# Kernel tuning notes

Hardware: AMD Instinct MI355X
Metric: run time of the kernel (lower is better)

## Reference

```python
import jax, jax.numpy as jnp
import numpy as np

B, S, D, T = 64, 1024, 768, 10
IS = int(S * 0.3)   # 307, token-mix inner dim
ID = int(D * 0.3)   # 230, channel-mix inner dim
EPS = 1e-5


def _cond_ln(x, embed, tid):
    # LayerNorm over last dim (no affine), then per-sample gamma/beta
    mu = jnp.mean(x, axis=-1, keepdims=True)
    var = jnp.mean(jnp.square(x - mu), axis=-1, keepdims=True)
    out = (x - mu) / jnp.sqrt(var + EPS)
    gb = embed[tid]                      # [B, 2D]
    gamma, beta = gb[:, :D], gb[:, D:]
    return gamma[:, None, :] * out + beta[:, None, :]


def setup_inputs() -> dict:
    key = jax.random.key(0)
    ks = jax.random.split(key, 8)
    x = jax.random.normal(ks[0], (B, S, D), dtype=jnp.float32)
    tasks_id = jax.random.randint(ks[1], (B,), 0, T)
    # conditional LN embeddings: gamma ~ N(1, 0.02), beta = 0
    cln1 = jnp.concatenate([1.0 + 0.02 * jax.random.normal(ks[2], (T, D)),
                            jnp.zeros((T, D))], axis=1).astype(jnp.float32)
    cln2 = jnp.concatenate([1.0 + 0.02 * jax.random.normal(ks[3], (T, D)),
                            jnp.zeros((T, D))], axis=1).astype(jnp.float32)
    # per-task weights stored [T, fout, fin] (kaiming-ish scale)
    w1_tok = jax.random.normal(ks[4], (T, IS, S), dtype=jnp.float32) * (2.0 / S) ** 0.5
    w2_tok = jax.random.normal(ks[5], (T, S, IS), dtype=jnp.float32) * (2.0 / IS) ** 0.5
    w1_ch = jax.random.normal(ks[6], (T, ID, D), dtype=jnp.float32) * (2.0 / D) ** 0.5
    w2_ch = jax.random.normal(ks[7], (T, D, ID), dtype=jnp.float32) * (2.0 / ID) ** 0.5
    return {"x": x, "tasks_id": tasks_id, "cln1": cln1, "cln2": cln2,
            "w1_tok": w1_tok, "w2_tok": w2_tok, "w1_ch": w1_ch, "w2_ch": w2_ch}


def reference(x, tasks_id, cln1, cln2, w1_tok, w2_tok, w1_ch, w2_ch):
    tid = tasks_id
    # --- token-mixing block (axis=1 ConditionalLinear) ---
    h = _cond_ln(x, cln1, tid)
    h = jnp.einsum('bnd,bcn->bcd', h, w1_tok[tid])   # [B, IS, D]
    h = jax.nn.gelu(h, approximate=False)
    h = jnp.einsum('bnd,bcn->bcd', h, w2_tok[tid])   # [B, S, D]
    x = x + h
    # --- channel-mixing block (axis=2 ConditionalLinear) ---
    h = _cond_ln(x, cln2, tid)
    h = jnp.einsum('bnd,bcd->bnc', h, w1_ch[tid])    # [B, S, ID]
    h = jax.nn.gelu(h, approximate=False)
    h = jnp.einsum('bnd,bcd->bnc', h, w2_ch[tid])    # [B, S, D]
    x = x + h
    return x
```

## Files before the change

### kernel.cpp

```cpp
#include <hip/hip_runtime.h>
#include <math.h>

typedef __bf16 bf16x8 __attribute__((ext_vector_type(8)));
typedef __bf16 bf16x4 __attribute__((ext_vector_type(4)));
typedef float  f32x4  __attribute__((ext_vector_type(4)));

constexpr int Bc = 64, Sc = 1024, Dc = 768;
constexpr int ISc = 307, IDc = 230;
constexpr int ISp = 384, IDp = 256;

static __device__ __forceinline__ float bf2f(unsigned short u) {
    return __builtin_bit_cast(float, (unsigned)u << 16);
}
static __device__ __forceinline__ float gelu_f(float v) {
    return 0.5f * v * (1.0f + erff(v * 0.70710678118654752f));
}

static __device__ __forceinline__ void gload16(const void* g, void* l) {
    __builtin_amdgcn_global_load_lds(
        (const __attribute__((address_space(1))) void*)g,
        (__attribute__((address_space(3))) void*)l, 16, 0, 0);
}

constexpr int CH0 = 10 * ISp * (Sc  / 8);
constexpr int CH1 = 10 * Sc  * (ISp / 8);
constexpr int CH2 = 10 * IDp * (Dc  / 8);
constexpr int CH3 = 10 * Dc  * (IDp / 8);
constexpr int CB0 = CH0, CB1 = CB0 + CH1, CB2 = CB1 + CH2, CB3 = CB2 + CH3;

__device__ __forceinline__ void cvt_one(
    const float* __restrict__ in, __bf16* __restrict__ out,
    int inrows, int outrows, int incols, int outcols, int c)
{
    const int cpr  = outcols >> 3;
    const int perT = outrows * cpr;
    const int t    = c / perT;
    const int rem  = c - t * perT;
    const int r    = rem / cpr;
    const int cc   = (rem - r * cpr) * 8;
    bf16x8 o;
    if (r < inrows) {
        const float* src = in + ((long)t * inrows + r) * incols + cc;
        #pragma unroll
        for (int e = 0; e < 8; e++)
            o[e] = (cc + e < incols) ? (__bf16)src[e] : (__bf16)0.0f;
    } else {
        #pragma unroll
        for (int e = 0; e < 8; e++) o[e] = (__bf16)0.0f;
    }
    *reinterpret_cast<bf16x8*>(out + ((long)t * outrows + r) * outcols + cc) = o;
}

__global__ __launch_bounds__(256) void cvt_all(
    const float* __restrict__ w1t, const float* __restrict__ w2t,
    const float* __restrict__ w1c, const float* __restrict__ w2c,
    __bf16* __restrict__ o1t, __bf16* __restrict__ o2t,
    __bf16* __restrict__ o1c, __bf16* __restrict__ o2c)
{
    const int c = blockIdx.x * 256 + threadIdx.x;
    if (c < CB0)      cvt_one(w1t, o1t, ISc, ISp, Sc,  Sc,  c);
    else if (c < CB1) cvt_one(w2t, o2t, Sc,  Sc,  ISc, ISp, c - CB0);
    else if (c < CB2) cvt_one(w1c, o1c, IDc, IDp, Dc,  Dc,  c - CB1);
    else if (c < CB3) cvt_one(w2c, o2c, Dc,  Dc,  IDc, IDp, c - CB2);
}

__global__ __launch_bounds__(256) void ln1_t(
    const float* __restrict__ x, const int* __restrict__ tasks,
    const float* __restrict__ cln, __bf16* __restrict__ h1T)
{
    constexpr int RPB = 32, LDT = Dc + 8;
    __shared__ unsigned short T[RPB * LDT];
    const int b   = blockIdx.y;
    const int t   = tasks[b];
    const int s0  = blockIdx.x * RPB;
    const int tid = threadIdx.x;
    const int wv  = tid >> 6;
    const int l   = tid & 63;

    const float4* Ga = reinterpret_cast<const float4*>(cln + (long)t * 2 * Dc);
    const float4* Be = reinterpret_cast<const float4*>(cln + (long)t * 2 * Dc + Dc);
    const float4 g0 = Ga[l], g1 = Ga[l + 64], g2 = Ga[l + 128];
    const float4 b0 = Be[l], b1 = Be[l + 64], b2 = Be[l + 128];

    #pragma unroll
    for (int rr = 0; rr < 8; rr++) {
        const int r = wv * 8 + rr;
        const float4* xr = reinterpret_cast<const float4*>(x + ((long)b * Sc + s0 + r) * Dc);
        const float4 v0 = xr[l], v1 = xr[l + 64], v2 = xr[l + 128];
        float s = v0.x + v0.y + v0.z + v0.w + v1.x + v1.y + v1.z + v1.w
                + v2.x + v2.y + v2.z + v2.w;
        float q = v0.x*v0.x + v0.y*v0.y + v0.z*v0.z + v0.w*v0.w
                + v1.x*v1.x + v1.y*v1.y + v1.z*v1.z + v1.w*v1.w
                + v2.x*v2.x + v2.y*v2.y + v2.z*v2.z + v2.w*v2.w;
        #pragma unroll
        for (int o = 1; o < 64; o <<= 1) { s += __shfl_xor(s, o); q += __shfl_xor(q, o); }
        const float mu   = s * (1.0f / Dc);
        const float var  = fmaxf(q * (1.0f / Dc) - mu * mu, 0.0f);
        const float rstd = 1.0f / sqrtf(var + 1e-5f);
        unsigned short* tr = &T[r * LDT];
        bf16x4 o0, o1, o2;
        o0[0] = (__bf16)(g0.x * ((v0.x - mu) * rstd) + b0.x);
        o0[1] = (__bf16)(g0.y * ((v0.y - mu) * rstd) + b0.y);
        o0[2] = (__bf16)(g0.z * ((v0.z - mu) * rstd) + b0.z);
        o0[3] = (__bf16)(g0.w * ((v0.w - mu) * rstd) + b0.w);
        o1[0] = (__bf16)(g1.x * ((v1.x - mu) * rstd) + b1.x);
        o1[1] = (__bf16)(g1.y * ((v1.y - mu) * rstd) + b1.y);
        o1[2] = (__bf16)(g1.z * ((v1.z - mu) * rstd) + b1.z);
        o1[3] = (__bf16)(g1.w * ((v1.w - mu) * rstd) + b1.w);
        o2[0] = (__bf16)(g2.x * ((v2.x - mu) * rstd) + b2.x);
        o2[1] = (__bf16)(g2.y * ((v2.y - mu) * rstd) + b2.y);
        o2[2] = (__bf16)(g2.z * ((v2.z - mu) * rstd) + b2.z);
        o2[3] = (__bf16)(g2.w * ((v2.w - mu) * rstd) + b2.w);
        *reinterpret_cast<bf16x4*>(&tr[l * 4])        = o0;
        *reinterpret_cast<bf16x4*>(&tr[256 + l * 4])  = o1;
        *reinterpret_cast<bf16x4*>(&tr[512 + l * 4])  = o2;
    }
    __syncthreads();
    #pragma unroll
    for (int c = 0; c < 3; c++) {
        const int d = tid + c * 256;
        unsigned short tmp[32];
        #pragma unroll
        for (int e = 0; e < 32; e++) tmp[e] = T[e * LDT + d];
        __bf16* dst = h1T + ((long)b * Dc + d) * Sc + s0;
        #pragma unroll
        for (int u = 0; u < 4; u++)
            reinterpret_cast<uint4*>(dst)[u] = reinterpret_cast<const uint4*>(tmp)[u];
    }
}

template<int DOGELU, int RESM, int OUTF32, int ATASK>
__global__ __launch_bounds__(256, 2) void gemm_tn(
    const __bf16* __restrict__ A, long sA, int lda,
    const __bf16* __restrict__ B, long sB, int ldb,
    const void* __restrict__ R, long sR,
    void* __restrict__ C, long sC, int ldc,
    const int* __restrict__ tasks, int M, int N, int K)
{
    constexpr int BM = 128, BN = 128, BK = 64;
    constexpr int BUFB = 32768;
    __shared__ uint4 lds4[2 * BUFB / 16];
    char* lbase = (char*)lds4;

    const int gx  = gridDim.x, gy = gridDim.y;
    const int tpb = gx * gy;
    const long lin = blockIdx.x + (long)gx * (blockIdx.y + (long)gy * blockIdx.z);
    const int  xcd  = (int)(lin & 7);
    const long idx  = lin >> 3;
    const int  lb   = (int)(idx / tpb);
    const int  tile = (int)(idx - (long)lb * tpb);
    const int  b    = xcd * 8 + lb;
    const int  m0   = (tile / gx) * BM;
    const int  n0   = (tile % gx) * BN;

    const int t = tasks[b];
    const __bf16* Ab = A + (ATASK ? (long)t : (long)b) * sA;
    const __bf16* Bb = B + (ATASK ? (long)b : (long)t) * sB;
    const int tid = threadIdx.x, lane = tid & 63, wid = tid >> 6;
    const int wm = (wid >> 1) * 64, wn = (wid & 1) * 64;
    const int l15 = lane & 15, l4 = lane >> 4;

    f32x4 acc[4][4];
    #pragma unroll
    for (int i = 0; i < 4; i++)
        #pragma unroll
        for (int j = 0; j < 4; j++)
            acc[i][j] = (f32x4){0.f, 0.f, 0.f, 0.f};

    auto STAGE = [&](int k0, int buf) {
        char* dst = lbase + buf * BUFB;
        #pragma unroll
        for (int rep = 0; rep < 4; rep++) {
            const int c = rep * 256 + tid;
            const int m = c >> 3, ch = c & 7;
            const int gk = k0 + ((ch ^ (m & 7)) << 3);
            gload16(Ab + (long)(m0 + m) * lda + gk, dst + c * 16);
        }
        #pragma unroll
        for (int rep = 0; rep < 4; rep++) {
            const int c = rep * 256 + tid;
            const int n = c >> 3, ch = c & 7;
            const int gk = k0 + ((ch ^ (n & 7)) << 3);
            gload16(Bb + (long)(n0 + n) * ldb + gk, dst + 16384 + c * 16);
        }
    };

    const int nt = K / BK;
    STAGE(0, 0);
    __syncthreads();
    int cur = 0;
    for (int tt = 0; tt < nt; tt++) {
        if (tt + 1 < nt) STAGE((tt + 1) * BK, cur ^ 1);
        const char* bb = lbase + cur * BUFB;
        #pragma unroll
        for (int h = 0; h < 2; h++) {
            bf16x8 af[4], bfr[4];
            #pragma unroll
            for (int i = 0; i < 4; i++) {
                const int row = wm + i * 16 + l15;
                af[i] = *reinterpret_cast<const bf16x8*>(
                    bb + row * 128 + (((h * 4 + l4) ^ (row & 7)) << 4));
            }
            #pragma unroll
            for (int j = 0; j < 4; j++) {
                const int row = wn + j * 16 + l15;
                bfr[j] = *reinterpret_cast<const bf16x8*>(
                    bb + 16384 + row * 128 + (((h * 4 + l4) ^ (row & 7)) << 4));
            }
            #pragma unroll
            for (int i = 0; i < 4; i++)
                #pragma unroll
                for (int j = 0; j < 4; j++)
                    acc[i][j] = __builtin_amdgcn_mfma_f32_16x16x32_bf16(af[i], bfr[j], acc[i][j], 0, 0, 0);
        }
        __syncthreads();
        cur ^= 1;
    }

    float*  Cf = (float*)C  + (long)b * sC;
    __bf16* Ch = (__bf16*)C + (long)b * sC;
    const float*  Rf = (RESM == 1) ? ((const float*)R  + (long)b * sR) : nullptr;
    const __bf16* Rh = (RESM == 2) ? ((const __bf16*)R + (long)b * sR) : nullptr;

    #pragma unroll
    for (int i = 0; i < 4; i++) {
        #pragma unroll
        for (int j = 0; j < 4; j++) {
            const int gn = n0 + wn + j * 16 + l15;
            #pragma unroll
            for (int r = 0; r < 4; r++) {
                const int gm = m0 + wm + i * 16 + l4 * 4 + r;
                float v = acc[i][j][r];
                if (DOGELU) v = gelu_f(v);
                if (RESM == 1) v += Rf[(long)gm * ldc + gn];
                if (RESM == 2) v += (float)Rh[(long)gm * ldc + gn];
                if (OUTF32) Cf[(long)gm * ldc + gn] = v;
                else        Ch[(long)gm * ldc + gn] = (__bf16)v;
            }
        }
    }
}

__global__ __launch_bounds__(256, 2) void mlp_ch(
    const __bf16* __restrict__ x1, const int* __restrict__ tasks,
    const float* __restrict__ cln2,
    const __bf16* __restrict__ wC1,
    const __bf16* __restrict__ wC2,
    float* __restrict__ out)
{
    __shared__ float2 st[64];
    __shared__ unsigned short G[64 * 256];
    __shared__ char sbuf[2][20480];

    const int lin = blockIdx.x;
    const int xcd = lin & 7;
    const int idx = lin >> 3;
    const int b   = xcd * 8 + (idx >> 4);
    const int m0  = (idx & 15) * 64;
    const int t   = tasks[b];

    const int tid = threadIdx.x;
    const int wid = tid >> 6, lane = tid & 63;
    const int wn  = wid * 64;
    const int l15 = lane & 15, l4 = lane >> 4;

    const __bf16* xb = x1 + ((long)b * Sc + m0) * Dc;
    const float*  cg = cln2 + (long)t * 2 * Dc;
    const float*  cb = cg + Dc;

    #pragma unroll 2
    for (int rr = 0; rr < 16; rr++) {
        const int m = wid * 16 + rr;
        const ushort4* xr = reinterpret_cast<const ushort4*>(xb + (long)m * Dc);
        const ushort4 u0 = xr[lane], u1 = xr[lane + 64], u2 = xr[lane + 128];
        float s = 0.f, q = 0.f, v;
        v = bf2f(u0.x); s += v; q += v*v;  v = bf2f(u0.y); s += v; q += v*v;
        v = bf2f(u0.z); s += v; q += v*v;  v = bf2f(u0.w); s += v; q += v*v;
        v = bf2f(u1.x); s += v; q += v*v;  v = bf2f(u1.y); s += v; q += v*v;
        v = bf2f(u1.z); s += v; q += v*v;  v = bf2f(u1.w); s += v; q += v*v;
        v = bf2f(u2.x); s += v; q += v*v;  v = bf2f(u2.y); s += v; q += v*v;
        v = bf2f(u2.z); s += v; q += v*v;  v = bf2f(u2.w); s += v; q += v*v;
        #pragma unroll
        for (int o = 1; o < 64; o <<= 1) { s += __shfl_xor(s, o); q += __shfl_xor(q, o); }
        if (lane == 0) {
            const float mu  = s * (1.0f / Dc);
            const float var = fmaxf(q * (1.0f / Dc) - mu * mu, 0.0f);
            st[m] = make_float2(mu, 1.0f / sqrtf(var + 1e-5f));
        }
    }
    __syncthreads();

    const int am = tid >> 2, ach = tid & 3;
    const float2 ams = st[am];
    const __bf16* arow = xb + (long)am * Dc;

    auto loadA = [&](int kt) -> bf16x8 {
        return *reinterpret_cast<const bf16x8*>(arow + kt * 32 + ach * 8);
    };
    auto writeA = [&](bf16x8 a, int buf) {
        *reinterpret_cast<bf16x8*>(sbuf[buf] + am * 64 + ((ach ^ (am & 3)) << 4)) = a;
    };
    auto stageB1 = [&](int kt, int buf) {
        #pragma unroll
        for (int rep = 0; rep < 4; rep++) {
            const int c = rep * 256 + tid;
            const int n = c >> 2, ch = c & 3;
            const int gk = kt * 32 + ((ch ^ (n & 3)) << 3);
            gload16(wC1 + ((long)t * IDp + n) * Dc + gk, sbuf[buf] + 4096 + c * 16);
        }
    };
    auto xformA = [&](bf16x8 raw, int kt) -> bf16x8 {
        const int gk = kt * 32 + ach * 8;
        const float4 ga0 = reinterpret_cast<const float4*>(cg + gk)[0];
        const float4 ga1 = reinterpret_cast<const float4*>(cg + gk)[1];
        const float4 be0 = reinterpret_cast<const float4*>(cb + gk)[0];
        const float4 be1 = reinterpret_cast<const float4*>(cb + gk)[1];
        bf16x8 o;
        o[0] = (__bf16)(ga0.x * ((float)raw[0] - ams.x) * ams.y + be0.x);
        o[1] = (__bf16)(ga0.y * ((float)raw[1] - ams.x) * ams.y + be0.y);
        o[2] = (__bf16)(ga0.z * ((float)raw[2] - ams.x) * ams.y + be0.z);
        o[3] = (__bf16)(ga0.w * ((float)raw[3] - ams.x) * ams.y + be0.w);
        o[4] = (__bf16)(ga1.x * ((float)raw[4] - ams.x) * ams.y + be1.x);
        o[5] = (__bf16)(ga1.y * ((float)raw[5] - ams.x) * ams.y + be1.y);
        o[6] = (__bf16)(ga1.z * ((float)raw[6] - ams.x) * ams.y + be1.z);
        o[7] = (__bf16)(ga1.w * ((float)raw[7] - ams.x) * ams.y + be1.w);
        return o;
    };

    f32x4 acc[4][4];
    #pragma unroll
    for (int i = 0; i < 4; i++)
        #pragma unroll
        for (int j = 0; j < 4; j++)
            acc[i][j] = (f32x4){0.f, 0.f, 0.f, 0.f};

    {
        bf16x8 a0 = loadA(0);
        stageB1(0, 0);
        writeA(xformA(a0, 0), 0);
        __syncthreads();
        for (int kt = 0; kt < 24; kt++) {
            const int buf = kt & 1;
            bf16x8 anx;
            if (kt < 23) { anx = loadA(kt + 1); stageB1(kt + 1, buf ^ 1); }
            const char* Abase = sbuf[buf];
            const char* Bbase = sbuf[buf] + 4096;
            bf16x8 af[4], bfr[4];
            #pragma unroll
            for (int i = 0; i < 4; i++) {
                const int row = i * 16 + l15;
                af[i] = *reinterpret_cast<const bf16x8*>(
                    Abase + row * 64 + ((l4 ^ (row & 3)) << 4));
            }
            #pragma unroll
            for (int j = 0; j < 4; j++) {
                const int row = wn + j * 16 + l15;
                bfr[j] = *reinterpret_cast<const bf16x8*>(
                    Bbase + row * 64 + ((l4 ^ (row & 3)) << 4));
            }
            #pragma unroll
            for (int i = 0; i < 4; i++)
                #pragma unroll
                for (int j = 0; j < 4; j++)
                    acc[i][j] = __builtin_amdgcn_mfma_f32_16x16x32_bf16(af[i], bfr[j], acc[i][j], 0, 0, 0);
            if (kt < 23) writeA(xformA(anx, kt + 1), buf ^ 1);
            __syncthreads();
        }
    }

    #pragma unroll
    for (int i = 0; i < 4; i++) {
        #pragma unroll
        for (int j = 0; j < 4; j++) {
            const int k = wn + j * 16 + l15;
            #pragma unroll
            for (int r = 0; r < 4; r++) {
                const int m = i * 16 + l4 * 4 + r;
                const float v = gelu_f(acc[i][j][r]);
                const int phys = (k >> 3) ^ (m & 7);
                G[m * 256 + phys * 8 + (k & 7)] =
                    __builtin_bit_cast(unsigned short, (__bf16)v);
            }
        }
    }
    __syncthreads();

    const __bf16* w2b = wC2 + (long)t * Dc * IDp;
    float* ob = out + ((long)b * Sc + m0) * Dc;
    for (int nc = 0; nc < 3; nc++) {
        auto stageB2 = [&](int kt, int buf) {
            #pragma unroll
            for (int rep = 0; rep < 4; rep++) {
                const int c = rep * 256 + tid;
                const int n = c >> 2, ch = c & 3;
                const int gk = kt * 32 + ((ch ^ (n & 3)) << 3);
                gload16(w2b + (long)(nc * 256 + n) * IDp + gk, sbuf[buf] + c * 16);
            }
        };
        f32x4 a2[4][4];
        #pragma unroll
        for (int i = 0; i < 4; i++)
            #pragma unroll
            for (int j = 0; j < 4; j++)
                a2[i][j] = (f32x4){0.f, 0.f, 0.f, 0.f};

        stageB2(0, 0);
        __syncthreads();
        for (int kt = 0; kt < 8; kt++) {
            const int buf = kt & 1;
            if (kt < 7) stageB2(kt + 1, buf ^ 1);
            bf16x8 af[4], bfr[4];
            #pragma unroll
            for (int i = 0; i < 4; i++) {
                const int row = i * 16 + l15;
                const int phys = (kt * 4 + l4) ^ (row & 7);
                af[i] = *reinterpret_cast<const bf16x8*>(
                    (const char*)G + row * 512 + phys * 16);
            }
            #pragma unroll
            for (int j = 0; j < 4; j++) {
                const int row = wn + j * 16 + l15;
                bfr[j] = *reinterpret_cast<const bf16x8*>(
                    sbuf[buf] + row * 64 + ((l4 ^ (row & 3)) << 4));
            }
            #pragma unroll
            for (int i = 0; i < 4; i++)
                #pragma unroll
                for (int j = 0; j < 4; j++)
                    a2[i][j] = __builtin_amdgcn_mfma_f32_16x16x32_bf16(af[i], bfr[j], a2[i][j], 0, 0, 0);
            __syncthreads();
        }
        #pragma unroll
        for (int i = 0; i < 4; i++) {
            #pragma unroll
            for (int j = 0; j < 4; j++) {
                const int gn = nc * 256 + wn + j * 16 + l15;
                #pragma unroll
                for (int r = 0; r < 4; r++) {
                    const int gm = i * 16 + l4 * 4 + r;
                    ob[(long)gm * Dc + gn] =
                        a2[i][j][r] + (float)xb[(long)gm * Dc + gn];
                }
            }
        }
    }
}

extern "C" void kernel_launch(void* const* d_in, const int* in_sizes, int n_in,
                              void* d_out, int out_size, void* d_ws, size_t ws_size,
                              hipStream_t stream) {
    const float* x      = (const float*)d_in[0];
    const int*   tasks  = (const int*)  d_in[1];
    const float* cln1   = (const float*)d_in[2];
    const float* cln2   = (const float*)d_in[3];
    const float* w1_tok = (const float*)d_in[4];
    const float* w2_tok = (const float*)d_in[5];
    const float* w1_ch  = (const float*)d_in[6];
    const float* w2_ch  = (const float*)d_in[7];
    float* out = (float*)d_out;

    char* ws = (char*)d_ws;
    const long oT1 = 0;
    const long oT2 = oT1 + (long)10 * ISp * Sc * 2;
    const long oC1 = oT2 + (long)10 * Sc * ISp * 2;
    const long oC2 = oC1 + (long)10 * IDp * Dc * 2;
    const long oA  = oC2 + (long)10 * Dc * IDp * 2;
    const long oG  = oA  + (long)Bc * Dc * Sc * 2;
    __bf16* wT1  = (__bf16*)(ws + oT1);
    __bf16* wT2  = (__bf16*)(ws + oT2);
    __bf16* wC1  = (__bf16*)(ws + oC1);
    __bf16* wC2  = (__bf16*)(ws + oC2);
    __bf16* h1T  = (__bf16*)(ws + oA);
    __bf16* x1   = (__bf16*)(ws + oA);
    __bf16* gbf  = (__bf16*)(ws + oG);

    const dim3 blk(256);
    auto cdiv = [](long a, long b) { return (int)((a + b - 1) / b); };

    cvt_all<<<cdiv(CB3, 256), blk, 0, stream>>>(
        w1_tok, w2_tok, w1_ch, w2_ch, wT1, wT2, wC1, wC2);

    ln1_t<<<dim3(Sc / 32, Bc), blk, 0, stream>>>(x, tasks, cln1, h1T);

    gemm_tn<1, 0, 0, 0><<<dim3(ISp / 128, Dc / 128, Bc), blk, 0, stream>>>(
        h1T, (long)Dc * Sc, Sc,
        wT1, (long)ISp * Sc, Sc,
        nullptr, 0,
        gbf, (long)Dc * ISp, ISp,
        tasks, Dc, ISp, Sc);

    gemm_tn<0, 1, 0, 1><<<dim3(Dc / 128, Sc / 128, Bc), blk, 0, stream>>>(
        wT2, (long)Sc * ISp, ISp,
        gbf, (long)Dc * ISp, ISp,
        x, (long)Sc * Dc,
        x1, (long)Sc * Dc, Dc,
        tasks, Sc, Dc, ISp);

    mlp_ch<<<(Sc / 64) * Bc, blk, 0, stream>>>(x1, tasks, cln2, wC1, wC2, out);
}
```

Before: 453.1 us.

## Double threads per block to 512 with eight waves splitting tiles

The tiled GEMM kernels and the fused channel-MLP kernel now launch 512 threads (8 waves) instead of 256. Each wave owns a 32-row sub-tile instead of 64 rows, and the staging and LN-transform loops are reshaped to match. This halves accumulator registers per wave and raises waves per CU, to hide latency better. The cost is less register-level reuse per wave: each wave loads B fragments for half as many MFMAs, so LDS read traffic per MFMA rises, and a larger block synchronises more waves.

```diff
diff --git a/kernel.cpp b/kernel.cpp
--- a/kernel.cpp
+++ b/kernel.cpp
@@ -130,7 +130,7 @@
 }
 
 template<int DOGELU, int RESM, int OUTF32, int ATASK>
-__global__ __launch_bounds__(256, 2) void gemm_tn(
+__global__ __launch_bounds__(512, 4) void gemm_tn(
     const __bf16* __restrict__ A, long sA, int lda,
     const __bf16* __restrict__ B, long sB, int ldb,
     const void* __restrict__ R, long sR,
@@ -157,12 +157,12 @@
     const __bf16* Ab = A + (ATASK ? (long)t : (long)b) * sA;
     const __bf16* Bb = B + (ATASK ? (long)b : (long)t) * sB;
     const int tid = threadIdx.x, lane = tid & 63, wid = tid >> 6;
-    const int wm = (wid >> 1) * 64, wn = (wid & 1) * 64;
+    const int wm = (wid >> 1) * 32, wn = (wid & 1) * 64;
     const int l15 = lane & 15, l4 = lane >> 4;
 
-    f32x4 acc[4][4];
-    #pragma unroll
-    for (int i = 0; i < 4; i++)
+    f32x4 acc[2][4];
+    #pragma unroll
+    for (int i = 0; i < 2; i++)
         #pragma unroll
         for (int j = 0; j < 4; j++)
             acc[i][j] = (f32x4){0.f, 0.f, 0.f, 0.f};
@@ -170,15 +170,15 @@
     auto STAGE = [&](int k0, int buf) {
         char* dst = lbase + buf * BUFB;
         #pragma unroll
-        for (int rep = 0; rep < 4; rep++) {
-            const int c = rep * 256 + tid;
+        for (int rep = 0; rep < 2; rep++) {
+            const int c = rep * 512 + tid;
             const int m = c >> 3, ch = c & 7;
             const int gk = k0 + ((ch ^ (m & 7)) << 3);
             gload16(Ab + (long)(m0 + m) * lda + gk, dst + c * 16);
         }
         #pragma unroll
-        for (int rep = 0; rep < 4; rep++) {
-            const int c = rep * 256 + tid;
+        for (int rep = 0; rep < 2; rep++) {
+            const int c = rep * 512 + tid;
             const int n = c >> 3, ch = c & 7;
             const int gk = k0 + ((ch ^ (n & 7)) << 3);
             gload16(Bb + (long)(n0 + n) * ldb + gk, dst + 16384 + c * 16);
@@ -194,9 +194,9 @@
         const char* bb = lbase + cur * BUFB;
         #pragma unroll
         for (int h = 0; h < 2; h++) {
-            bf16x8 af[4], bfr[4];
-            #pragma unroll
-            for (int i = 0; i < 4; i++) {
+            bf16x8 af[2], bfr[4];
+            #pragma unroll
+            for (int i = 0; i < 2; i++) {
                 const int row = wm + i * 16 + l15;
                 af[i] = *reinterpret_cast<const bf16x8*>(
                     bb + row * 128 + (((h * 4 + l4) ^ (row & 7)) << 4));
@@ -208,7 +208,7 @@
                     bb + 16384 + row * 128 + (((h * 4 + l4) ^ (row & 7)) << 4));
             }
             #pragma unroll
-            for (int i = 0; i < 4; i++)
+            for (int i = 0; i < 2; i++)
                 #pragma unroll
                 for (int j = 0; j < 4; j++)
                     acc[i][j] = __builtin_amdgcn_mfma_f32_16x16x32_bf16(af[i], bfr[j], acc[i][j], 0, 0, 0);
@@ -223,7 +223,7 @@
     const __bf16* Rh = (RESM == 2) ? ((const __bf16*)R + (long)b * sR) : nullptr;
 
     #pragma unroll
-    for (int i = 0; i < 4; i++) {
+    for (int i = 0; i < 2; i++) {
         #pragma unroll
         for (int j = 0; j < 4; j++) {
             const int gn = n0 + wn + j * 16 + l15;
@@ -241,7 +241,7 @@
     }
 }
 
-__global__ __launch_bounds__(256, 2) void mlp_ch(
+__global__ __launch_bounds__(512, 4) void mlp_ch(
     const __bf16* __restrict__ x1, const int* __restrict__ tasks,
     const float* __restrict__ cln2,
     const __bf16* __restrict__ wC1,
@@ -261,7 +261,7 @@
 
     const int tid = threadIdx.x;
     const int wid = tid >> 6, lane = tid & 63;
-    const int wn  = wid * 64;
+    const int wm  = (wid >> 2) * 32, wn = (wid & 3) * 64;
     const int l15 = lane & 15, l4 = lane >> 4;
 
     const __bf16* xb = x1 + ((long)b * Sc + m0) * Dc;
@@ -269,8 +269,8 @@
     const float*  cb = cg + Dc;
 
     #pragma unroll 2
-    for (int rr = 0; rr < 16; rr++) {
-        const int m = wid * 16 + rr;
+    for (int rr = 0; rr < 8; rr++) {
+        const int m = wid * 8 + rr;
         const ushort4* xr = reinterpret_cast<const ushort4*>(xb + (long)m * Dc);
         const ushort4 u0 = xr[lane], u1 = xr[lane + 64], u2 = xr[lane + 128];
         float s = 0.f, q = 0.f, v;
@@ -290,65 +290,61 @@
     }
     __syncthreads();
 
-    const int am = tid >> 2, ach = tid & 3;
+    const int am = tid >> 3, ach8 = tid & 7;
     const float2 ams = st[am];
     const __bf16* arow = xb + (long)am * Dc;
 
-    auto loadA = [&](int kt) -> bf16x8 {
-        return *reinterpret_cast<const bf16x8*>(arow + kt * 32 + ach * 8);
+    auto loadA = [&](int kt) -> bf16x4 {
+        return *reinterpret_cast<const bf16x4*>(arow + kt * 32 + ach8 * 4);
     };
-    auto writeA = [&](bf16x8 a, int buf) {
-        *reinterpret_cast<bf16x8*>(sbuf[buf] + am * 64 + ((ach ^ (am & 3)) << 4)) = a;
+    auto writeA = [&](bf16x4 a, int buf) {
+        const int phys = (ach8 >> 1) ^ (am & 3);
+        *reinterpret_cast<bf16x4*>(
+            sbuf[buf] + am * 64 + (phys << 4) + (ach8 & 1) * 8) = a;
     };
     auto stageB1 = [&](int kt, int buf) {
         #pragma unroll
-        for (int rep = 0; rep < 4; rep++) {
-            const int c = rep * 256 + tid;
+        for (int rep = 0; rep < 2; rep++) {
+            const int c = rep * 512 + tid;
             const int n = c >> 2, ch = c & 3;
             const int gk = kt * 32 + ((ch ^ (n & 3)) << 3);
             gload16(wC1 + ((long)t * IDp + n) * Dc + gk, sbuf[buf] + 4096 + c * 16);
         }
     };
-    auto xformA = [&](bf16x8 raw, int kt) -> bf16x8 {
-        const int gk = kt * 32 + ach * 8;
-        const float4 ga0 = reinterpret_cast<const float4*>(cg + gk)[0];
-        const float4 ga1 = reinterpret_cast<const float4*>(cg + gk)[1];
-        const float4 be0 = reinterpret_cast<const float4*>(cb + gk)[0];
-        const float4 be1 = reinterpret_cast<const float4*>(cb + gk)[1];
-        bf16x8 o;
-        o[0] = (__bf16)(ga0.x * ((float)raw[0] - ams.x) * ams.y + be0.x);
-        o[1] = (__bf16)(ga0.y * ((float)raw[1] - ams.x) * ams.y + be0.y);
-        o[2] = (__bf16)(ga0.z * ((float)raw[2] - ams.x) * ams.y + be0.z);
-        o[3] = (__bf16)(ga0.w * ((float)raw[3] - ams.x) * ams.y + be0.w);
-        o[4] = (__bf16)(ga1.x * ((float)raw[4] - ams.x) * ams.y + be1.x);
-        o[5] = (__bf16)(ga1.y * ((float)raw[5] - ams.x) * ams.y + be1.y);
-        o[6] = (__bf16)(ga1.z * ((float)raw[6] - ams.x) * ams.y + be1.z);
-        o[7] = (__bf16)(ga1.w * ((float)raw[7] - ams.x) * ams.y + be1.w);
+    auto xformA = [&](bf16x4 raw, int kt) -> bf16x4 {
+        const int gk = kt * 32 + ach8 * 4;
+        const float4 ga = *reinterpret_cast<const float4*>(cg + gk);
+        const float4 be = *reinterpret_cast<const float4*>(cb + gk);
+        bf16x4 o;
+        o[0] = (__bf16)(ga.x * ((float)raw[0] - ams.x) * ams.y + be.x);
+        o[1] = (__bf16)(ga.y * ((float)raw[1] - ams.x) * ams.y + be.y);
+        o[2] = (__bf16)(ga.z * ((float)raw[2] - ams.x) * ams.y + be.z);
+        o[3] = (__bf16)(ga.w * ((float)raw[3] - ams.x) * ams.y + be.w);
         return o;
     };
 
-    f32x4 acc[4][4];
-    #pragma unroll
-    for (int i = 0; i < 4; i++)
+    f32x4 acc[2][4];
+    #pragma unroll
+    for (int i = 0; i < 2; i++)
         #pragma unroll
         for (int j = 0; j < 4; j++)
             acc[i][j] = (f32x4){0.f, 0.f, 0.f, 0.f};
 
     {
-        bf16x8 a0 = loadA(0);
+        bf16x4 a0 = loadA(0);
         stageB1(0, 0);
         writeA(xformA(a0, 0), 0);
         __syncthreads();
         for (int kt = 0; kt < 24; kt++) {
             const int buf = kt & 1;
-            bf16x8 anx;
+            bf16x4 anx;
             if (kt < 23) { anx = loadA(kt + 1); stageB1(kt + 1, buf ^ 1); }
             const char* Abase = sbuf[buf];
             const char* Bbase = sbuf[buf] + 4096;
-            bf16x8 af[4], bfr[4];
-            #pragma unroll
-            for (int i = 0; i < 4; i++) {
-                const int row = i * 16 + l15;
+            bf16x8 af[2], bfr[4];
+            #pragma unroll
+            for (int i = 0; i < 2; i++) {
+                const int row = wm + i * 16 + l15;
                 af[i] = *reinterpret_cast<const bf16x8*>(
                     Abase + row * 64 + ((l4 ^ (row & 3)) << 4));
             }
@@ -359,7 +355,7 @@
                     Bbase + row * 64 + ((l4 ^ (row & 3)) << 4));
             }
             #pragma unroll
-            for (int i = 0; i < 4; i++)
+            for (int i = 0; i < 2; i++)
                 #pragma unroll
                 for (int j = 0; j < 4; j++)
                     acc[i][j] = __builtin_amdgcn_mfma_f32_16x16x32_bf16(af[i], bfr[j], acc[i][j], 0, 0, 0);
@@ -369,13 +365,13 @@
     }
 
     #pragma unroll
-    for (int i = 0; i < 4; i++) {
+    for (int i = 0; i < 2; i++) {
         #pragma unroll
         for (int j = 0; j < 4; j++) {
             const int k = wn + j * 16 + l15;
             #pragma unroll
             for (int r = 0; r < 4; r++) {
-                const int m = i * 16 + l4 * 4 + r;
+                const int m = wm + i * 16 + l4 * 4 + r;
                 const float v = gelu_f(acc[i][j][r]);
                 const int phys = (k >> 3) ^ (m & 7);
                 G[m * 256 + phys * 8 + (k & 7)] =
@@ -390,16 +386,16 @@
     for (int nc = 0; nc < 3; nc++) {
         auto stageB2 = [&](int kt, int buf) {
             #pragma unroll
-            for (int rep = 0; rep < 4; rep++) {
-                const int c = rep * 256 + tid;
+            for (int rep = 0; rep < 2; rep++) {
+                const int c = rep * 512 + tid;
                 const int n = c >> 2, ch = c & 3;
                 const int gk = kt * 32 + ((ch ^ (n & 3)) << 3);
                 gload16(w2b + (long)(nc * 256 + n) * IDp + gk, sbuf[buf] + c * 16);
             }
         };
-        f32x4 a2[4][4];
-        #pragma unroll
-        for (int i = 0; i < 4; i++)
+        f32x4 a2[2][4];
+        #pragma unroll
+        for (int i = 0; i < 2; i++)
             #pragma unroll
             for (int j = 0; j < 4; j++)
                 a2[i][j] = (f32x4){0.f, 0.f, 0.f, 0.f};
@@ -409,10 +405,10 @@
         for (int kt = 0; kt < 8; kt++) {
             const int buf = kt & 1;
             if (kt < 7) stageB2(kt + 1, buf ^ 1);
-            bf16x8 af[4], bfr[4];
-            #pragma unroll
-            for (int i = 0; i < 4; i++) {
-                const int row = i * 16 + l15;
+            bf16x8 af[2], bfr[4];
+            #pragma unroll
+            for (int i = 0; i < 2; i++) {
+                const int row = wm + i * 16 + l15;
                 const int phys = (kt * 4 + l4) ^ (row & 7);
                 af[i] = *reinterpret_cast<const bf16x8*>(
                     (const char*)G + row * 512 + phys * 16);
@@ -424,20 +420,20 @@
                     sbuf[buf] + row * 64 + ((l4 ^ (row & 3)) << 4));
             }
             #pragma unroll
-            for (int i = 0; i < 4; i++)
+            for (int i = 0; i < 2; i++)
                 #pragma unroll
                 for (int j = 0; j < 4; j++)
                     a2[i][j] = __builtin_amdgcn_mfma_f32_16x16x32_bf16(af[i], bfr[j], a2[i][j], 0, 0, 0);
             __syncthreads();
         }
         #pragma unroll
-        for (int i = 0; i < 4; i++) {
+        for (int i = 0; i < 2; i++) {
             #pragma unroll
             for (int j = 0; j < 4; j++) {
                 const int gn = nc * 256 + wn + j * 16 + l15;
                 #pragma unroll
                 for (int r = 0; r < 4; r++) {
-                    const int gm = i * 16 + l4 * 4 + r;
+                    const int gm = wm + i * 16 + l4 * 4 + r;
                     ob[(long)gm * Dc + gn] =
                         a2[i][j][r] + (float)xb[(long)gm * Dc + gn];
                 }
@@ -482,19 +478,19 @@
 
     ln1_t<<<dim3(Sc / 32, Bc), blk, 0, stream>>>(x, tasks, cln1, h1T);
 
-    gemm_tn<1, 0, 0, 0><<<dim3(ISp / 128, Dc / 128, Bc), blk, 0, stream>>>(
+    gemm_tn<1, 0, 0, 0><<<dim3(ISp / 128, Dc / 128, Bc), 512, 0, stream>>>(
         h1T, (long)Dc * Sc, Sc,
         wT1, (long)ISp * Sc, Sc,
         nullptr, 0,
         gbf, (long)Dc * ISp, ISp,
         tasks, Dc, ISp, Sc);
 
-    gemm_tn<0, 1, 0, 1><<<dim3(Dc / 128, Sc / 128, Bc), blk, 0, stream>>>(
+    gemm_tn<0, 1, 0, 1><<<dim3(Dc / 128, Sc / 128, Bc), 512, 0, stream>>>(
         wT2, (long)Sc * ISp, ISp,
         gbf, (long)Dc * ISp, ISp,
         x, (long)Sc * Dc,
         x1, (long)Sc * Dc, Dc,
         tasks, Sc, Dc, ISp);
 
-    mlp_ch<<<(Sc / 64) * Bc, blk, 0, stream>>>(x1, tasks, cln2, wC1, wC2, out);
-}
+    mlp_ch<<<(Sc / 64) * Bc, 512, 0, stream>>>(x1, tasks, cln2, wC1, wC2, out);
+}
```

Result: faster. 437.0 us (-3.6%).
